# Kernel optimization log

Hardware: AMD Instinct MI355X
Metric: run time of the kernel (lower is better)

The kernel has to match this reference:

```python
import jax, jax.numpy as jnp
import numpy as np

EPS = 1e-07


def setup_inputs() -> dict:
    key = jax.random.key(0)
    k1, k2, k3, k4, k5, k6 = jax.random.split(key, 6)
    B, S, E = 128, 512, 64  # batch, seq_len == n_items, emb_size
    user_emb = jax.random.normal(k1, (B, S, E), dtype=jnp.float32)
    item_emb = jax.random.normal(k2, (B, S, E), dtype=jnp.float32)
    cluster_weights = jax.random.uniform(k3, (B, S, 1), dtype=jnp.float32)
    # binary keep-mask over sequence positions (multiplicative)
    last_item_mask = (jax.random.uniform(k4, (B, 1, S)) > 0.5).astype(jnp.float32)
    proj_w = jax.random.normal(k5, (1, 1), dtype=jnp.float32)
    proj_b = jax.random.normal(k6, (1,), dtype=jnp.float32)
    return {
        "user_emb": user_emb,
        "item_emb": item_emb,
        "cluster_weights": cluster_weights,
        "last_item_mask": last_item_mask,
        "proj_w": proj_w,
        "proj_b": proj_b,
    }


def reference(user_emb, item_emb, cluster_weights, last_item_mask, proj_w, proj_b):
    # L2-normalize with clamped norm (matches torch.clamp(norm, 1e-7))
    u = user_emb / jnp.maximum(jnp.linalg.norm(user_emb, axis=-1, keepdims=True), EPS)
    v = item_emb / jnp.maximum(jnp.linalg.norm(item_emb, axis=-1, keepdims=True), EPS)
    # cosine sim: [B, n_items, seq_len] (n_items == seq_len == S)
    cos = jnp.einsum("bse,bne->bns", u, v)
    # cluster_weights [B,S,1] broadcasts over the seq_len axis, indexed by dim1
    # (faithful to torch broadcast of [B,N,S,1] * [B,S,1,1] with N == S)
    sims = cos * cluster_weights  # [B,N,S]
    # Linear(1,1) + sigmoid applied elementwise (scalar affine)
    sims = jax.nn.sigmoid(sims * proj_w[0, 0] + proj_b[0])
    # permute to [B, seq_len, n_items], mask [B,1,S] broadcasts over last axis
    sims = jnp.swapaxes(sims, 1, 2) * last_item_mask
    # max over dim 2 -> [B, seq_len]
    return jnp.max(sims, axis=2)
```

## Files before the change

kernel.cpp:

```cpp
#include <hip/hip_runtime.h>
#include <math.h>

#define B_ 128
#define S_ 512
#define E_ 64
#define PAD_ 72

typedef short bf16x8 __attribute__((ext_vector_type(8)));
typedef float f32x4 __attribute__((ext_vector_type(4)));

__device__ __forceinline__ unsigned short f2bf(float f) {
  union { float f; unsigned int u; } v; v.f = f;
  unsigned int u = v.u;
  return (unsigned short)((u + 0x7fffu + ((u >> 16) & 1u)) >> 16);
}

__global__ __launch_bounds__(512) void fused_kernel(
    const float* __restrict__ ue, const float* __restrict__ ve,
    const float* __restrict__ cw, const float* __restrict__ mask,
    const float* __restrict__ pw, const float* __restrict__ pb,
    float* __restrict__ out) {
  __shared__ unsigned short vlds[S_ * PAD_];
  __shared__ unsigned short ulds[256 * PAD_];

  const int b = blockIdx.x >> 1;
  const int shalf = blockIdx.x & 1;
  const int tid = threadIdx.x;
  const int wv = tid >> 6;
  const int lane = tid & 63;
  const int c = lane & 15;
  const int g = lane >> 4;

  const float w0 = pw[0];
  const float* __restrict__ vb = ve + (size_t)b * S_ * E_;
  const float* __restrict__ cwb = cw + (size_t)b * S_;
  const float* __restrict__ ub = ue + ((size_t)b * S_ + shalf * 256) * E_;

#pragma unroll 4
  for (int i = 0; i < 16; ++i) {
    int row = wv * 64 + i * 4 + g;
    f32x4 x = *(const f32x4*)(vb + (size_t)row * E_ + c * 4);
    float ss = x[0] * x[0] + x[1] * x[1] + x[2] * x[2] + x[3] * x[3];
    ss += __shfl_xor(ss, 1); ss += __shfl_xor(ss, 2);
    ss += __shfl_xor(ss, 4); ss += __shfl_xor(ss, 8);
    float scale = (1.0f / fmaxf(sqrtf(ss), 1e-7f)) * w0 * cwb[row];
    ushort4 p;
    p.x = f2bf(x[0] * scale); p.y = f2bf(x[1] * scale);
    p.z = f2bf(x[2] * scale); p.w = f2bf(x[3] * scale);
    *(ushort4*)(vlds + (size_t)row * PAD_ + c * 4) = p;
  }
#pragma unroll 4
  for (int i = 0; i < 8; ++i) {
    int row = wv * 32 + i * 4 + g;
    f32x4 x = *(const f32x4*)(ub + (size_t)row * E_ + c * 4);
    float ss = x[0] * x[0] + x[1] * x[1] + x[2] * x[2] + x[3] * x[3];
    ss += __shfl_xor(ss, 1); ss += __shfl_xor(ss, 2);
    ss += __shfl_xor(ss, 4); ss += __shfl_xor(ss, 8);
    float scale = 1.0f / fmaxf(sqrtf(ss), 1e-7f);
    ushort4 p;
    p.x = f2bf(x[0] * scale); p.y = f2bf(x[1] * scale);
    p.z = f2bf(x[2] * scale); p.w = f2bf(x[3] * scale);
    *(ushort4*)(ulds + (size_t)row * PAD_ + c * 4) = p;
  }

  const float* __restrict__ mb = mask + (size_t)b * S_;
  unsigned int mbits = 0;
#pragma unroll
  for (int i = 0; i < 32; ++i)
    mbits |= (mb[i * 16 + c] > 0.5f ? 1u : 0u) << i;

  __syncthreads();

  const unsigned short* ur = ulds + (size_t)(wv * 32 + c) * PAD_ + g * 8;
  bf16x8 a00 = *(const bf16x8*)(ur);
  bf16x8 a01 = *(const bf16x8*)(ur + 32);
  bf16x8 a10 = *(const bf16x8*)(ur + 16 * PAD_);
  bf16x8 a11 = *(const bf16x8*)(ur + 16 * PAD_ + 32);

  float r0[4] = {-INFINITY, -INFINITY, -INFINITY, -INFINITY};
  float r1[4] = {-INFINITY, -INFINITY, -INFINITY, -INFINITY};

#pragma unroll 4
  for (int it = 0; it < 32; ++it) {
    const unsigned short* vr = vlds + (size_t)(it * 16 + c) * PAD_ + g * 8;
    bf16x8 b0 = *(const bf16x8*)(vr);
    bf16x8 b1 = *(const bf16x8*)(vr + 32);
    f32x4 acc0 = {0.f, 0.f, 0.f, 0.f};
    f32x4 acc1 = {0.f, 0.f, 0.f, 0.f};
    acc0 = __builtin_amdgcn_mfma_f32_16x16x32_bf16(a00, b0, acc0, 0, 0, 0);
    acc0 = __builtin_amdgcn_mfma_f32_16x16x32_bf16(a01, b1, acc0, 0, 0, 0);
    acc1 = __builtin_amdgcn_mfma_f32_16x16x32_bf16(a10, b0, acc1, 0, 0, 0);
    acc1 = __builtin_amdgcn_mfma_f32_16x16x32_bf16(a11, b1, acc1, 0, 0, 0);
    bool keep = (mbits >> it) & 1u;
#pragma unroll
    for (int i = 0; i < 4; ++i) {
      r0[i] = fmaxf(r0[i], keep ? acc0[i] : -INFINITY);
      r1[i] = fmaxf(r1[i], keep ? acc1[i] : -INFINITY);
    }
  }

#pragma unroll
  for (int i = 0; i < 4; ++i) {
    float v = r0[i];
    v = fmaxf(v, __shfl_xor(v, 1)); v = fmaxf(v, __shfl_xor(v, 2));
    v = fmaxf(v, __shfl_xor(v, 4)); v = fmaxf(v, __shfl_xor(v, 8));
    r0[i] = v;
    v = r1[i];
    v = fmaxf(v, __shfl_xor(v, 1)); v = fmaxf(v, __shfl_xor(v, 2));
    v = fmaxf(v, __shfl_xor(v, 4)); v = fmaxf(v, __shfl_xor(v, 8));
    r1[i] = v;
  }

  if (c == 0) {
    float bias = pb[0];
    size_t base = (size_t)b * S_ + shalf * 256 + wv * 32;
#pragma unroll
    for (int i = 0; i < 4; ++i) {
      float v = r0[i];
      out[base + g * 4 + i] =
          (v < -1e30f) ? 0.0f : 1.0f / (1.0f + expf(-(v + bias)));
      v = r1[i];
      out[base + 16 + g * 4 + i] =
          (v < -1e30f) ? 0.0f : 1.0f / (1.0f + expf(-(v + bias)));
    }
  }
}

extern "C" void kernel_launch(void* const* d_in, const int* in_sizes, int n_in,
                              void* d_out, int out_size, void* d_ws, size_t ws_size,
                              hipStream_t stream) {
  const float* ue = (const float*)d_in[0];
  const float* ve = (const float*)d_in[1];
  const float* cw = (const float*)d_in[2];
  const float* mask = (const float*)d_in[3];
  const float* pw = (const float*)d_in[4];
  const float* pb = (const float*)d_in[5];
  float* out = (float*)d_out;

  hipLaunchKernelGGL(fused_kernel, dim3(2 * B_), dim3(512), 0, stream,
                     ue, ve, cw, mask, pw, pb, out);
}
```

Measured before the change: 21.12 us.

## Use 1024-thread blocks with 2D wave tiling and fold mask into MFMA accumulator

Doubles threads per block and splits waves into a 4x4 grid over user rows and item tiles, so each wave reuses its B fragments across four A subtiles and then combines partial maxima through shared memory. The mask becomes an additive penalty loaded into the MFMA initial accumulator, which removes the per-element selects. Global loads are hoisted into registers ahead of normalization to raise memory-level parallelism, and block indices are remapped to spread batches across XCDs. The cost is an extra barrier and shared-memory reduction step, plus higher register pressure at 1024 threads.

```diff
diff --git a/kernel.cpp b/kernel.cpp
--- a/kernel.cpp
+++ b/kernel.cpp
@@ -15,44 +15,68 @@
   return (unsigned short)((u + 0x7fffu + ((u >> 16) & 1u)) >> 16);
 }
 
-__global__ __launch_bounds__(512) void fused_kernel(
+__global__ __launch_bounds__(1024) void fused_kernel(
     const float* __restrict__ ue, const float* __restrict__ ve,
     const float* __restrict__ cw, const float* __restrict__ mask,
     const float* __restrict__ pw, const float* __restrict__ pb,
     float* __restrict__ out) {
   __shared__ unsigned short vlds[S_ * PAD_];
   __shared__ unsigned short ulds[256 * PAD_];
+  __shared__ float comb[4][256];
 
-  const int b = blockIdx.x >> 1;
-  const int shalf = blockIdx.x & 1;
+  const int bx = blockIdx.x;
+  const int b = (bx & 7) * 16 + ((bx >> 3) >> 1);
+  const int shalf = (bx >> 3) & 1;
+
   const int tid = threadIdx.x;
   const int wv = tid >> 6;
   const int lane = tid & 63;
   const int c = lane & 15;
   const int g = lane >> 4;
+  const int ws = wv >> 2;
+  const int wn = wv & 3;
 
   const float w0 = pw[0];
   const float* __restrict__ vb = ve + (size_t)b * S_ * E_;
   const float* __restrict__ cwb = cw + (size_t)b * S_;
   const float* __restrict__ ub = ue + ((size_t)b * S_ + shalf * 256) * E_;
+  const float* __restrict__ mb = mask + (size_t)b * S_;
 
-#pragma unroll 4
-  for (int i = 0; i < 16; ++i) {
-    int row = wv * 64 + i * 4 + g;
-    f32x4 x = *(const f32x4*)(vb + (size_t)row * E_ + c * 4);
+  f32x4 vs[8];
+  float cws[8];
+#pragma unroll
+  for (int i = 0; i < 8; ++i) {
+    int row = wv * 32 + i * 4 + g;
+    vs[i] = *(const f32x4*)(vb + (size_t)row * E_ + c * 4);
+    cws[i] = cwb[row];
+  }
+  f32x4 us[4];
+#pragma unroll
+  for (int i = 0; i < 4; ++i) {
+    int row = wv * 16 + i * 4 + g;
+    us[i] = *(const f32x4*)(ub + (size_t)row * E_ + c * 4);
+  }
+  float pen[8];
+#pragma unroll
+  for (int j = 0; j < 8; ++j)
+    pen[j] = (mb[(wn * 8 + j) * 16 + c] > 0.5f) ? 0.0f : -1e30f;
+
+#pragma unroll
+  for (int i = 0; i < 8; ++i) {
+    f32x4 x = vs[i];
     float ss = x[0] * x[0] + x[1] * x[1] + x[2] * x[2] + x[3] * x[3];
     ss += __shfl_xor(ss, 1); ss += __shfl_xor(ss, 2);
     ss += __shfl_xor(ss, 4); ss += __shfl_xor(ss, 8);
-    float scale = (1.0f / fmaxf(sqrtf(ss), 1e-7f)) * w0 * cwb[row];
+    float scale = (1.0f / fmaxf(sqrtf(ss), 1e-7f)) * w0 * cws[i];
     ushort4 p;
     p.x = f2bf(x[0] * scale); p.y = f2bf(x[1] * scale);
     p.z = f2bf(x[2] * scale); p.w = f2bf(x[3] * scale);
+    int row = wv * 32 + i * 4 + g;
     *(ushort4*)(vlds + (size_t)row * PAD_ + c * 4) = p;
   }
-#pragma unroll 4
-  for (int i = 0; i < 8; ++i) {
-    int row = wv * 32 + i * 4 + g;
-    f32x4 x = *(const f32x4*)(ub + (size_t)row * E_ + c * 4);
+#pragma unroll
+  for (int i = 0; i < 4; ++i) {
+    f32x4 x = us[i];
     float ss = x[0] * x[0] + x[1] * x[1] + x[2] * x[2] + x[3] * x[3];
     ss += __shfl_xor(ss, 1); ss += __shfl_xor(ss, 2);
     ss += __shfl_xor(ss, 4); ss += __shfl_xor(ss, 8);
@@ -60,69 +84,70 @@
     ushort4 p;
     p.x = f2bf(x[0] * scale); p.y = f2bf(x[1] * scale);
     p.z = f2bf(x[2] * scale); p.w = f2bf(x[3] * scale);
+    int row = wv * 16 + i * 4 + g;
     *(ushort4*)(ulds + (size_t)row * PAD_ + c * 4) = p;
   }
 
-  const float* __restrict__ mb = mask + (size_t)b * S_;
-  unsigned int mbits = 0;
-#pragma unroll
-  for (int i = 0; i < 32; ++i)
-    mbits |= (mb[i * 16 + c] > 0.5f ? 1u : 0u) << i;
-
   __syncthreads();
 
-  const unsigned short* ur = ulds + (size_t)(wv * 32 + c) * PAD_ + g * 8;
-  bf16x8 a00 = *(const bf16x8*)(ur);
-  bf16x8 a01 = *(const bf16x8*)(ur + 32);
-  bf16x8 a10 = *(const bf16x8*)(ur + 16 * PAD_);
-  bf16x8 a11 = *(const bf16x8*)(ur + 16 * PAD_ + 32);
+  const unsigned short* urp = ulds + (size_t)(ws * 64 + c) * PAD_ + g * 8;
+  bf16x8 a[4][2];
+#pragma unroll
+  for (int st = 0; st < 4; ++st) {
+    a[st][0] = *(const bf16x8*)(urp + st * 16 * PAD_);
+    a[st][1] = *(const bf16x8*)(urp + st * 16 * PAD_ + 32);
+  }
 
-  float r0[4] = {-INFINITY, -INFINITY, -INFINITY, -INFINITY};
-  float r1[4] = {-INFINITY, -INFINITY, -INFINITY, -INFINITY};
+  float r[4][4];
+#pragma unroll
+  for (int st = 0; st < 4; ++st)
+#pragma unroll
+    for (int i = 0; i < 4; ++i) r[st][i] = -INFINITY;
 
-#pragma unroll 4
-  for (int it = 0; it < 32; ++it) {
+#pragma unroll
+  for (int j = 0; j < 8; ++j) {
+    int it = wn * 8 + j;
     const unsigned short* vr = vlds + (size_t)(it * 16 + c) * PAD_ + g * 8;
     bf16x8 b0 = *(const bf16x8*)(vr);
     bf16x8 b1 = *(const bf16x8*)(vr + 32);
-    f32x4 acc0 = {0.f, 0.f, 0.f, 0.f};
-    f32x4 acc1 = {0.f, 0.f, 0.f, 0.f};
-    acc0 = __builtin_amdgcn_mfma_f32_16x16x32_bf16(a00, b0, acc0, 0, 0, 0);
-    acc0 = __builtin_amdgcn_mfma_f32_16x16x32_bf16(a01, b1, acc0, 0, 0, 0);
-    acc1 = __builtin_amdgcn_mfma_f32_16x16x32_bf16(a10, b0, acc1, 0, 0, 0);
-    acc1 = __builtin_amdgcn_mfma_f32_16x16x32_bf16(a11, b1, acc1, 0, 0, 0);
-    bool keep = (mbits >> it) & 1u;
+    f32x4 ci = {pen[j], pen[j], pen[j], pen[j]};
 #pragma unroll
-    for (int i = 0; i < 4; ++i) {
-      r0[i] = fmaxf(r0[i], keep ? acc0[i] : -INFINITY);
-      r1[i] = fmaxf(r1[i], keep ? acc1[i] : -INFINITY);
+    for (int st = 0; st < 4; ++st) {
+      f32x4 acc = __builtin_amdgcn_mfma_f32_16x16x32_bf16(a[st][0], b0, ci, 0, 0, 0);
+      acc = __builtin_amdgcn_mfma_f32_16x16x32_bf16(a[st][1], b1, acc, 0, 0, 0);
+      r[st][0] = fmaxf(r[st][0], acc[0]);
+      r[st][1] = fmaxf(r[st][1], acc[1]);
+      r[st][2] = fmaxf(r[st][2], acc[2]);
+      r[st][3] = fmaxf(r[st][3], acc[3]);
     }
   }
 
 #pragma unroll
-  for (int i = 0; i < 4; ++i) {
-    float v = r0[i];
-    v = fmaxf(v, __shfl_xor(v, 1)); v = fmaxf(v, __shfl_xor(v, 2));
-    v = fmaxf(v, __shfl_xor(v, 4)); v = fmaxf(v, __shfl_xor(v, 8));
-    r0[i] = v;
-    v = r1[i];
-    v = fmaxf(v, __shfl_xor(v, 1)); v = fmaxf(v, __shfl_xor(v, 2));
-    v = fmaxf(v, __shfl_xor(v, 4)); v = fmaxf(v, __shfl_xor(v, 8));
-    r1[i] = v;
+  for (int st = 0; st < 4; ++st)
+#pragma unroll
+    for (int i = 0; i < 4; ++i) {
+      float v = r[st][i];
+      v = fmaxf(v, __shfl_xor(v, 1)); v = fmaxf(v, __shfl_xor(v, 2));
+      v = fmaxf(v, __shfl_xor(v, 4)); v = fmaxf(v, __shfl_xor(v, 8));
+      r[st][i] = v;
+    }
+
+  if (c == 0) {
+#pragma unroll
+    for (int st = 0; st < 4; ++st)
+#pragma unroll
+      for (int i = 0; i < 4; ++i)
+        comb[wn][ws * 64 + st * 16 + g * 4 + i] = r[st][i];
   }
 
-  if (c == 0) {
+  __syncthreads();
+
+  if (tid < 256) {
+    float v = fmaxf(fmaxf(comb[0][tid], comb[1][tid]),
+                    fmaxf(comb[2][tid], comb[3][tid]));
     float bias = pb[0];
-    size_t base = (size_t)b * S_ + shalf * 256 + wv * 32;
-#pragma unroll
-    for (int i = 0; i < 4; ++i) {
-      float v = r0[i];
-      out[base + g * 4 + i] =
-          (v < -1e30f) ? 0.0f : 1.0f / (1.0f + expf(-(v + bias)));
-      v = r1[i];
-      out[base + 16 + g * 4 + i] =
-          (v < -1e30f) ? 0.0f : 1.0f / (1.0f + expf(-(v + bias)));
-    }
+    out[(size_t)b * S_ + shalf * 256 + tid] =
+        (v < -1e29f) ? 0.0f : 1.0f / (1.0f + expf(-(v + bias)));
   }
 }
 
@@ -137,6 +162,6 @@
   const float* pb = (const float*)d_in[5];
   float* out = (float*)d_out;
 
-  hipLaunchKernelGGL(fused_kernel, dim3(2 * B_), dim3(512), 0, stream,
+  hipLaunchKernelGGL(fused_kernel, dim3(2 * B_), dim3(1024), 0, stream,
                      ue, ve, cw, mask, pw, pb, out);
 }
```

Result: faster. 18.80 us (-11.0%).
